# Performance work log

Hardware: AMD Instinct MI355X
Metric: run time of the kernel (lower is better)

The kernel has to match this reference:

```python
import jax, jax.numpy as jnp
import numpy as np

EMBED = 768
HEADS = 12


def setup_inputs() -> dict:
    key = jax.random.key(0)
    k1, k2, k3, k4, k5 = jax.random.split(key, 5)
    B, N, E = 8, 1024, EMBED
    x = jax.random.normal(k1, (B, N, E), dtype=jnp.float32)
    # torch Linear stored as [in, out] here (math-equivalent: y = x @ W + b)
    w_qkv = jax.random.normal(k2, (E, 3 * E), dtype=jnp.float32) * (E ** -0.5)
    b_qkv = jax.random.normal(k3, (3 * E,), dtype=jnp.float32) * 0.02
    w_proj = jax.random.normal(k4, (E, E), dtype=jnp.float32) * (E ** -0.5)
    b_proj = jax.random.normal(k5, (E,), dtype=jnp.float32) * 0.02
    return {"x": x, "w_qkv": w_qkv, "b_qkv": b_qkv, "w_proj": w_proj, "b_proj": b_proj}


def reference(x, w_qkv, b_qkv, w_proj, b_proj):
    B, N, E = x.shape
    H = HEADS
    D = E // H
    qkv = x @ w_qkv + b_qkv                       # [B, N, 3E]
    # rearrange 'b n (h d qkv) -> qkv b h n d': qkv index is innermost in last dim
    qkv = qkv.reshape(B, N, H, D, 3)
    qkv = jnp.transpose(qkv, (4, 0, 2, 1, 3))      # [3, B, H, N, D]
    q, k, v = qkv[0], qkv[1], qkv[2]
    energy = jnp.einsum('bhqd,bhkd->bhqk', q, k)   # [B, H, N, N]
    scaling = float(E) ** 0.5
    # NOTE: original scales AFTER softmax (unusual but faithful)
    att = jax.nn.softmax(energy, axis=-1) / scaling
    # dropout_prob = 0.0 -> identity
    out = jnp.einsum('bhqk,bhkd->bhqd', att, v)    # [B, H, N, D]
    out = jnp.transpose(out, (0, 2, 1, 3)).reshape(B, N, E)
    return out @ w_proj + b_proj
```

## Files before the change

kernel.cpp:

```cpp
#include <hip/hip_runtime.h>
#include <hip/hip_bf16.h>
#include <stdint.h>

#define NSEQ 1024
#define EMB 768
#define HEADS 12
#define HD 64
#define BATCH 8
#define BHN (BATCH*HEADS)

typedef __attribute__((ext_vector_type(8))) short bf16x8;
typedef __attribute__((ext_vector_type(4))) short bf16x4;
typedef __attribute__((ext_vector_type(4))) float f32x4;

typedef const void __attribute__((address_space(1))) cglobal_void;
typedef void __attribute__((address_space(3))) lds_void_t;

#define LOG2E 1.4426950408889634f

__device__ __forceinline__ void load_lds16(const void* g, void* l) {
    __builtin_amdgcn_global_load_lds((cglobal_void*)g, (lds_void_t*)l, 16, 0, 0);
}

__device__ __forceinline__ unsigned short f2bf(float f) {
    __hip_bfloat16 h = __float2bfloat16(f);
    return *reinterpret_cast<unsigned short*>(&h);
}

__device__ __forceinline__ float exp2_hw(float x) {
#if __has_builtin(__builtin_amdgcn_exp2f)
    return __builtin_amdgcn_exp2f(x);
#else
    return exp2f(x);
#endif
}

__global__ void conv_x_kernel(const float* __restrict__ x, unsigned short* __restrict__ xb) {
    int i = (blockIdx.x * 256 + threadIdx.x) * 4;
    float4 v = *reinterpret_cast<const float4*>(x + i);
    ushort4 o;
    o.x = f2bf(v.x); o.y = f2bf(v.y); o.z = f2bf(v.z); o.w = f2bf(v.w);
    *reinterpret_cast<ushort4*>(xb + i) = o;
}

template <int PERM>
__global__ void transpose_w_kernel(const float* __restrict__ w, unsigned short* __restrict__ wt,
                                   int K, int C) {
    __shared__ unsigned short tile[64][65];
    int c0 = blockIdx.x * 64;
    int k0 = blockIdx.y * 64;
    int t = threadIdx.x;
    int r = t >> 2, cc = (t & 3) * 16;
#pragma unroll
    for (int e = 0; e < 16; e += 4) {
        float4 v = *reinterpret_cast<const float4*>(w + (size_t)(k0 + r) * C + c0 + cc + e);
        float s0 = (PERM && ((c0 + cc + e + 0) % 3 == 0)) ? LOG2E : 1.0f;
        float s1 = (PERM && ((c0 + cc + e + 1) % 3 == 0)) ? LOG2E : 1.0f;
        float s2 = (PERM && ((c0 + cc + e + 2) % 3 == 0)) ? LOG2E : 1.0f;
        float s3 = (PERM && ((c0 + cc + e + 3) % 3 == 0)) ? LOG2E : 1.0f;
        tile[r][cc + e + 0] = f2bf(v.x * s0);
        tile[r][cc + e + 1] = f2bf(v.y * s1);
        tile[r][cc + e + 2] = f2bf(v.z * s2);
        tile[r][cc + e + 3] = f2bf(v.w * s3);
    }
    __syncthreads();
    int c = t >> 2, kk0 = (t & 3) * 16;
    int cg = c0 + c;
    int n;
    if (PERM) {
        int qkv = cg % 3, h = cg / 192, d = (cg % 192) / 3;
        n = qkv * EMB + h * HD + d;
    } else {
        n = cg;
    }
    uint4 lo, hi;
    lo.x = (unsigned)tile[kk0 + 0][c] | ((unsigned)tile[kk0 + 1][c] << 16);
    lo.y = (unsigned)tile[kk0 + 2][c] | ((unsigned)tile[kk0 + 3][c] << 16);
    lo.z = (unsigned)tile[kk0 + 4][c] | ((unsigned)tile[kk0 + 5][c] << 16);
    lo.w = (unsigned)tile[kk0 + 6][c] | ((unsigned)tile[kk0 + 7][c] << 16);
    hi.x = (unsigned)tile[kk0 + 8][c] | ((unsigned)tile[kk0 + 9][c] << 16);
    hi.y = (unsigned)tile[kk0 + 10][c] | ((unsigned)tile[kk0 + 11][c] << 16);
    hi.z = (unsigned)tile[kk0 + 12][c] | ((unsigned)tile[kk0 + 13][c] << 16);
    hi.w = (unsigned)tile[kk0 + 14][c] | ((unsigned)tile[kk0 + 15][c] << 16);
    *reinterpret_cast<uint4*>(wt + (size_t)n * K + k0 + kk0) = lo;
    *reinterpret_cast<uint4*>(wt + (size_t)n * K + k0 + kk0 + 8) = hi;
}

__global__ void perm_bias_kernel(const float* __restrict__ b, float* __restrict__ bp) {
    int c = blockIdx.x * 256 + threadIdx.x;
    int qkv = c % 3, h = c / 192, d = (c % 192) / 3;
    bp[qkv * EMB + h * HD + d] = (qkv == 0) ? b[c] * LOG2E : b[c];
}

template <int MODE>
__launch_bounds__(256, 2)
__global__ void gemm_bt_kernel(const unsigned short* __restrict__ A,
                               const unsigned short* __restrict__ Bt,
                               const float* __restrict__ bias,
                               float* __restrict__ out,
                               unsigned short* __restrict__ qout,
                               unsigned short* __restrict__ kout,
                               unsigned short* __restrict__ vout,
                               int M, int N, int K, int tiles_n) {
    __shared__ unsigned short lds_a[128 * 64];
    __shared__ unsigned short lds_b[128 * 64];
    int bx = blockIdx.x;
    int tm = bx / tiles_n, tn = bx % tiles_n;
    int m0 = tm * 128, n0 = tn * 128;
    int t = threadIdx.x;
    int l = t & 63;
    int wr = (t >> 7) & 1, wc = (t >> 6) & 1;
    int wbase = (t & 192);

    f32x4 acc[4][4];
#pragma unroll
    for (int i = 0; i < 4; i++)
#pragma unroll
        for (int j = 0; j < 4; j++)
#pragma unroll
            for (int r = 0; r < 4; r++) acc[i][j][r] = 0.f;

    for (int kt = 0; kt < K; kt += 64) {
        __syncthreads();
#pragma unroll
        for (int i = 0; i < 4; i++) {
            int c = i * 256 + t;
            int row = c >> 3;
            int sc = ((c & 7) ^ (row & 7)) * 8;
            load_lds16(A + (size_t)(m0 + row) * K + kt + sc, lds_a + (size_t)(i * 256 + wbase) * 8);
            load_lds16(Bt + (size_t)(n0 + row) * K + kt + sc, lds_b + (size_t)(i * 256 + wbase) * 8);
        }
        __syncthreads();
#pragma unroll
        for (int kk = 0; kk < 2; kk++) {
            int cb = kk * 64 + (l >> 4) * 16;
            bf16x8 af[4], bfr[4];
#pragma unroll
            for (int i = 0; i < 4; i++) {
                int row = wr * 64 + i * 16 + (l & 15);
                af[i] = *reinterpret_cast<const bf16x8*>(
                    (const char*)lds_a + row * 128 + (cb ^ ((row & 7) << 4)));
            }
#pragma unroll
            for (int j = 0; j < 4; j++) {
                int row = wc * 64 + j * 16 + (l & 15);
                bfr[j] = *reinterpret_cast<const bf16x8*>(
                    (const char*)lds_b + row * 128 + (cb ^ ((row & 7) << 4)));
            }
#pragma unroll
            for (int i = 0; i < 4; i++)
#pragma unroll
                for (int j = 0; j < 4; j++) {
                    if (MODE == 2)
                        acc[i][j] = __builtin_amdgcn_mfma_f32_16x16x32_bf16(bfr[j], af[i], acc[i][j], 0, 0, 0);
                    else
                        acc[i][j] = __builtin_amdgcn_mfma_f32_16x16x32_bf16(af[i], bfr[j], acc[i][j], 0, 0, 0);
                }
        }
    }

    if (MODE == 2) {
#pragma unroll
        for (int j = 0; j < 4; j++) {
#pragma unroll
            for (int r = 0; r < 4; r++) {
                int nv = wc * 64 + j * 16 + ((l >> 4) * 4) + r + n0;
                float bv = bias[nv];
                int hh = nv >> 6, dd = nv & 63;
#pragma unroll
                for (int i = 0; i < 4; i++) {
                    int m_g = m0 + wr * 64 + i * 16 + (l & 15);
                    int bb = m_g >> 10, nn = m_g & 1023;
                    int nnp = (nn & ~31) | ((nn & 12) << 1) | ((nn >> 2) & 4) | (nn & 3);
                    vout[((size_t)(bb * HEADS + hh) * HD + dd) * NSEQ + nnp] =
                        f2bf(acc[i][j][r] + bv);
                }
            }
        }
    } else {
#pragma unroll
        for (int i = 0; i < 4; i++) {
            int mbase = m0 + wr * 64 + i * 16 + ((l >> 4) * 4);
#pragma unroll
            for (int j = 0; j < 4; j++) {
                int n_g = n0 + wc * 64 + j * 16 + (l & 15);
                float bv = bias[n_g];
#pragma unroll
                for (int r = 0; r < 4; r++) {
                    int m_g = mbase + r;
                    float v = acc[i][j][r] + bv;
                    if (MODE == 0) {
                        int rem = n_g - ((n_g >= 768) ? 768 : 0);
                        int hh = rem >> 6, dd = rem & 63;
                        int bb = m_g >> 10, nn = m_g & 1023;
                        if (n_g < 768)
                            qout[(size_t)((bb * HEADS + hh) * NSEQ + nn) * HD + dd] = f2bf(v);
                        else
                            kout[(size_t)((bb * HEADS + hh) * NSEQ + nn) * HD + dd] = f2bf(v);
                    } else {
                        out[(size_t)m_g * N + n_g] = v;
                    }
                }
            }
        }
    }
}

__launch_bounds__(256, 3)
__global__ void attn_kernel(const unsigned short* __restrict__ Q,
                            const unsigned short* __restrict__ K,
                            const unsigned short* __restrict__ Vt,
                            unsigned short* __restrict__ Oout) {
    __shared__ unsigned short k_lds[2][64 * 64];
    __shared__ unsigned short vt_lds[2][64 * 64];
    int bx = blockIdx.x;
    int bh = bx % BHN;
    int q0 = (bx / BHN) << 7;
    int b = bh / HEADS, h = bh % HEADS;
    int t = threadIdx.x, w = t >> 6, l = t & 63;
    int g = l >> 4, c16 = l & 15;
    const unsigned short* Qh = Q + (size_t)bh * NSEQ * HD;
    const unsigned short* Kh = K + (size_t)bh * NSEQ * HD;
    const unsigned short* Vth = Vt + (size_t)bh * NSEQ * HD;

    int qrA = q0 + w * 32 + c16;
    int qrB = qrA + 16;
    bf16x8 qfA[2], qfB[2];
    qfA[0] = *reinterpret_cast<const bf16x8*>(Qh + (size_t)qrA * HD + g * 8);
    qfA[1] = *reinterpret_cast<const bf16x8*>(Qh + (size_t)qrA * HD + 32 + g * 8);
    qfB[0] = *reinterpret_cast<const bf16x8*>(Qh + (size_t)qrB * HD + g * 8);
    qfB[1] = *reinterpret_cast<const bf16x8*>(Qh + (size_t)qrB * HD + 32 + g * 8);

    float lA = 0.f, lB = 0.f;
    f32x4 accA[4], accB[4];
#pragma unroll
    for (int jd = 0; jd < 4; jd++)
#pragma unroll
        for (int r = 0; r < 4; r++) { accA[jd][r] = 0.f; accB[jd][r] = 0.f; }

    auto stage = [&](int buf, int kv) {
#pragma unroll
        for (int i = 0; i < 2; i++) {
            int tt = i * 256 + t;
            int row = tt >> 3;
            int sc = ((tt & 7) ^ (row & 7)) * 8;
            load_lds16(Kh + (size_t)(kv + row) * HD + sc, k_lds[buf] + (size_t)(tt & ~63) * 8);
            load_lds16(Vth + (size_t)row * NSEQ + kv + sc, vt_lds[buf] + (size_t)(tt & ~63) * 8);
        }
    };

    stage(0, 0);
    __syncthreads();
    int cur = 0;
    for (int it = 0; it < 16; ++it) {
        if (it < 15) stage(cur ^ 1, (it + 1) << 6);

        const char* kbase = (const char*)k_lds[cur];
        const char* vbase = (const char*)vt_lds[cur];

        f32x4 stA[4], stB[4];
#pragma unroll
        for (int jk = 0; jk < 4; jk++)
#pragma unroll
            for (int r = 0; r < 4; r++) { stA[jk][r] = 0.f; stB[jk][r] = 0.f; }
        __builtin_amdgcn_s_setprio(1);
#pragma unroll
        for (int kk = 0; kk < 2; kk++) {
            int cb = kk * 64 + g * 16;
#pragma unroll
            for (int jk = 0; jk < 4; jk++) {
                int row = jk * 16 + c16;
                bf16x8 kf = *reinterpret_cast<const bf16x8*>(
                    kbase + row * 128 + (cb ^ ((row & 7) << 4)));
                stA[jk] = __builtin_amdgcn_mfma_f32_16x16x32_bf16(kf, qfA[kk], stA[jk], 0, 0, 0);
                stB[jk] = __builtin_amdgcn_mfma_f32_16x16x32_bf16(kf, qfB[kk], stB[jk], 0, 0, 0);
            }
        }
        __builtin_amdgcn_s_setprio(0);

#pragma unroll
        for (int jk = 0; jk < 4; jk++)
#pragma unroll
            for (int r = 0; r < 4; r++) {
                stA[jk][r] = exp2_hw(stA[jk][r]);
                stB[jk][r] = exp2_hw(stB[jk][r]);
            }

        bf16x8 pfA[2], pfB[2];
#pragma unroll
        for (int r = 0; r < 4; r++) {
            pfA[0][r] = (short)f2bf(stA[0][r]); pfA[0][4 + r] = (short)f2bf(stA[1][r]);
            pfA[1][r] = (short)f2bf(stA[2][r]); pfA[1][4 + r] = (short)f2bf(stA[3][r]);
            pfB[0][r] = (short)f2bf(stB[0][r]); pfB[0][4 + r] = (short)f2bf(stB[1][r]);
            pfB[1][r] = (short)f2bf(stB[2][r]); pfB[1][4 + r] = (short)f2bf(stB[3][r]);
        }

        __builtin_amdgcn_s_setprio(1);
#pragma unroll
        for (int ks = 0; ks < 2; ks++) {
            int cb = ks * 64 + g * 16;
#pragma unroll
            for (int jd = 0; jd < 4; jd++) {
                int row = jd * 16 + c16;
                bf16x8 vf = *reinterpret_cast<const bf16x8*>(
                    vbase + row * 128 + (cb ^ ((row & 7) << 4)));
                accA[jd] = __builtin_amdgcn_mfma_f32_16x16x32_bf16(vf, pfA[ks], accA[jd], 0, 0, 0);
                accB[jd] = __builtin_amdgcn_mfma_f32_16x16x32_bf16(vf, pfB[ks], accB[jd], 0, 0, 0);
            }
        }
        __builtin_amdgcn_s_setprio(0);

        float psA = (((stA[0][0] + stA[0][1]) + (stA[0][2] + stA[0][3])) +
                     ((stA[1][0] + stA[1][1]) + (stA[1][2] + stA[1][3]))) +
                    (((stA[2][0] + stA[2][1]) + (stA[2][2] + stA[2][3])) +
                     ((stA[3][0] + stA[3][1]) + (stA[3][2] + stA[3][3])));
        float psB = (((stB[0][0] + stB[0][1]) + (stB[0][2] + stB[0][3])) +
                     ((stB[1][0] + stB[1][1]) + (stB[1][2] + stB[1][3]))) +
                    (((stB[2][0] + stB[2][1]) + (stB[2][2] + stB[2][3])) +
                     ((stB[3][0] + stB[3][1]) + (stB[3][2] + stB[3][3])));
        psA += __shfl_xor(psA, 16);
        psA += __shfl_xor(psA, 32);
        psB += __shfl_xor(psB, 16);
        psB += __shfl_xor(psB, 32);
        lA += psA;
        lB += psB;

        __syncthreads();
        cur ^= 1;
    }

    const float scale = 27.712812921102035f;
    float invA = 1.0f / (lA * scale);
    float invB = 1.0f / (lB * scale);
    size_t qbaseA = ((size_t)(b * NSEQ + qrA) * HEADS + h) * HD;
    size_t qbaseB = ((size_t)(b * NSEQ + qrB) * HEADS + h) * HD;
#pragma unroll
    for (int jd = 0; jd < 4; jd++)
#pragma unroll
        for (int r = 0; r < 4; r++) {
            int d = jd * 16 + g * 4 + r;
            Oout[qbaseA + d] = f2bf(accA[jd][r] * invA);
            Oout[qbaseB + d] = f2bf(accB[jd][r] * invB);
        }
}

extern "C" void kernel_launch(void* const* d_in, const int* in_sizes, int n_in,
                              void* d_out, int out_size, void* d_ws, size_t ws_size,
                              hipStream_t stream) {
    const float* x = (const float*)d_in[0];
    const float* w_qkv = (const float*)d_in[1];
    const float* b_qkv = (const float*)d_in[2];
    const float* w_proj = (const float*)d_in[3];
    const float* b_proj = (const float*)d_in[4];

    char* ws = (char*)d_ws;
    unsigned short* xb      = (unsigned short*)(ws + 0);
    unsigned short* wt_qkv  = (unsigned short*)(ws + 12582912);
    unsigned short* wt_proj = (unsigned short*)(ws + 16121856);
    float*          biasp   = (float*)(ws + 17301504);
    unsigned short* qb      = (unsigned short*)(ws + 17310720);
    unsigned short* kb      = (unsigned short*)(ws + 29893632);
    unsigned short* vtb     = (unsigned short*)(ws + 42476544);
    unsigned short* ao      = (unsigned short*)(ws + 55059456);

    conv_x_kernel<<<6144, 256, 0, stream>>>(x, xb);
    transpose_w_kernel<1><<<dim3(36, 12), 256, 0, stream>>>(w_qkv, wt_qkv, EMB, 3 * EMB);
    transpose_w_kernel<0><<<dim3(12, 12), 256, 0, stream>>>(w_proj, wt_proj, EMB, EMB);
    perm_bias_kernel<<<9, 256, 0, stream>>>(b_qkv, biasp);

    gemm_bt_kernel<0><<<64 * 12, 256, 0, stream>>>(xb, wt_qkv, biasp, nullptr, qb, kb, nullptr,
                                                   8192, 3 * EMB, EMB, 12);
    gemm_bt_kernel<2><<<64 * 6, 256, 0, stream>>>(xb, wt_qkv + (size_t)1536 * EMB, biasp + 1536,
                                                  nullptr, nullptr, nullptr, vtb,
                                                  8192, 3 * EMB, EMB, 6);
    attn_kernel<<<BHN * 8, 256, 0, stream>>>(qb, kb, vtb, ao);
    gemm_bt_kernel<1><<<64 * 6, 256, 0, stream>>>(ao, wt_proj, b_proj, (float*)d_out,
                                                  nullptr, nullptr, nullptr,
                                                  8192, EMB, EMB, 6);
}
```

Baseline: 114.2 us.

## Merge QK and V projection GEMMs into one launch with XCD-aware block remap

The separate Q/K GEMM launch and V GEMM launch are folded into a single launch of 64x18 tiles, where tiles with tn>=12 take the V path (swapped MFMA operands, transposed permuted store). Block indices are remapped so consecutive tiles land on the same XCD chunk for better L2 reuse, and K/N become compile-time constants. This removes one kernel launch and the tail of the smaller V grid, filling the GPU with a single larger grid. It adds a per-block runtime branch on vpath in the inner loop.

After: 113.7 us. No clear change (-0.5%).

```diff
diff --git a/kernel.cpp b/kernel.cpp
--- a/kernel.cpp
+++ b/kernel.cpp
@@ -100,13 +100,21 @@
                                float* __restrict__ out,
                                unsigned short* __restrict__ qout,
                                unsigned short* __restrict__ kout,
-                               unsigned short* __restrict__ vout,
-                               int M, int N, int K, int tiles_n) {
+                               unsigned short* __restrict__ vout) {
+    constexpr int TN = (MODE == 0) ? 18 : 6;
+    constexpr int NWG = 64 * TN;
+    constexpr int CHUNK = NWG / 8;
+    constexpr int K = EMB;
     __shared__ unsigned short lds_a[128 * 64];
     __shared__ unsigned short lds_b[128 * 64];
-    int bx = blockIdx.x;
-    int tm = bx / tiles_n, tn = bx % tiles_n;
-    int m0 = tm * 128, n0 = tn * 128;
+    int bx0 = blockIdx.x;
+    int bx = (bx0 % 8) * CHUNK + bx0 / 8;
+    int tm = bx / TN, tn = bx % TN;
+    bool vpath = (MODE == 0) && (tn >= 12);
+    const unsigned short* Bt_eff = Bt + (vpath ? (size_t)1536 * K : (size_t)0);
+    const float* bias_eff = bias + (vpath ? 1536 : 0);
+    int n0 = (vpath ? tn - 12 : tn) * 128;
+    int m0 = tm * 128;
     int t = threadIdx.x;
     int l = t & 63;
     int wr = (t >> 7) & 1, wc = (t >> 6) & 1;
@@ -128,7 +136,7 @@
             int row = c >> 3;
             int sc = ((c & 7) ^ (row & 7)) * 8;
             load_lds16(A + (size_t)(m0 + row) * K + kt + sc, lds_a + (size_t)(i * 256 + wbase) * 8);
-            load_lds16(Bt + (size_t)(n0 + row) * K + kt + sc, lds_b + (size_t)(i * 256 + wbase) * 8);
+            load_lds16(Bt_eff + (size_t)(n0 + row) * K + kt + sc, lds_b + (size_t)(i * 256 + wbase) * 8);
         }
         __syncthreads();
 #pragma unroll
@@ -147,25 +155,29 @@
                 bfr[j] = *reinterpret_cast<const bf16x8*>(
                     (const char*)lds_b + row * 128 + (cb ^ ((row & 7) << 4)));
             }
-#pragma unroll
-            for (int i = 0; i < 4; i++)
-#pragma unroll
-                for (int j = 0; j < 4; j++) {
-                    if (MODE == 2)
+            if (vpath) {
+#pragma unroll
+                for (int i = 0; i < 4; i++)
+#pragma unroll
+                    for (int j = 0; j < 4; j++)
                         acc[i][j] = __builtin_amdgcn_mfma_f32_16x16x32_bf16(bfr[j], af[i], acc[i][j], 0, 0, 0);
-                    else
+            } else {
+#pragma unroll
+                for (int i = 0; i < 4; i++)
+#pragma unroll
+                    for (int j = 0; j < 4; j++)
                         acc[i][j] = __builtin_amdgcn_mfma_f32_16x16x32_bf16(af[i], bfr[j], acc[i][j], 0, 0, 0);
-                }
-        }
-    }
-
-    if (MODE == 2) {
+            }
+        }
+    }
+
+    if (vpath) {
 #pragma unroll
         for (int j = 0; j < 4; j++) {
 #pragma unroll
             for (int r = 0; r < 4; r++) {
                 int nv = wc * 64 + j * 16 + ((l >> 4) * 4) + r + n0;
-                float bv = bias[nv];
+                float bv = bias_eff[nv];
                 int hh = nv >> 6, dd = nv & 63;
 #pragma unroll
                 for (int i = 0; i < 4; i++) {
@@ -184,7 +196,7 @@
 #pragma unroll
             for (int j = 0; j < 4; j++) {
                 int n_g = n0 + wc * 64 + j * 16 + (l & 15);
-                float bv = bias[n_g];
+                float bv = bias_eff[n_g];
 #pragma unroll
                 for (int r = 0; r < 4; r++) {
                     int m_g = mbase + r;
@@ -198,7 +210,7 @@
                         else
                             kout[(size_t)((bb * HEADS + hh) * NSEQ + nn) * HD + dd] = f2bf(v);
                     } else {
-                        out[(size_t)m_g * N + n_g] = v;
+                        out[(size_t)m_g * EMB + n_g] = v;
                     }
                 }
             }
@@ -368,13 +380,8 @@
     transpose_w_kernel<0><<<dim3(12, 12), 256, 0, stream>>>(w_proj, wt_proj, EMB, EMB);
     perm_bias_kernel<<<9, 256, 0, stream>>>(b_qkv, biasp);
 
-    gemm_bt_kernel<0><<<64 * 12, 256, 0, stream>>>(xb, wt_qkv, biasp, nullptr, qb, kb, nullptr,
-                                                   8192, 3 * EMB, EMB, 12);
-    gemm_bt_kernel<2><<<64 * 6, 256, 0, stream>>>(xb, wt_qkv + (size_t)1536 * EMB, biasp + 1536,
-                                                  nullptr, nullptr, nullptr, vtb,
-                                                  8192, 3 * EMB, EMB, 6);
+    gemm_bt_kernel<0><<<64 * 18, 256, 0, stream>>>(xb, wt_qkv, biasp, nullptr, qb, kb, vtb);
     attn_kernel<<<BHN * 8, 256, 0, stream>>>(qb, kb, vtb, ao);
     gemm_bt_kernel<1><<<64 * 6, 256, 0, stream>>>(ao, wt_proj, b_proj, (float*)d_out,
-                                                  nullptr, nullptr, nullptr,
-                                                  8192, EMB, EMB, 6);
-}
+                                                  nullptr, nullptr, nullptr);
+}
```
